# Kernel tuning notes

Hardware: AMD Instinct MI355X
Metric: run time of the kernel (lower is better)

## Reference

```python
import jax, jax.numpy as jnp
import numpy as np

B, N = 512, 128
NFEAT, NHID, NHEADS, HID = 133, 60, 8, 300
FP_DIM, FP2, TASK = 1489, 512, 1
ALPHA = 0.2
NEG = -9e15


def _lin(k, fi, fo):
    s = 1.0 / np.sqrt(fi)
    return jax.random.uniform(k, (fi, fo), minval=-s, maxval=s, dtype=jnp.float32)


def _vec(k, fi, n):
    s = 1.0 / np.sqrt(fi)
    return jax.random.uniform(k, (n,), minval=-s, maxval=s, dtype=jnp.float32)


def setup_inputs() -> dict:
    key = jax.random.key(0)
    ks = jax.random.split(key, 24)
    x = jax.random.normal(ks[0], (B, N, NFEAT), dtype=jnp.float32)
    adj = jax.random.randint(ks[1], (B, N, N), 0, 2, dtype=jnp.int32)
    adj = jnp.maximum(adj, jnp.eye(N, dtype=jnp.int32)[None])  # ensure valid softmax rows
    fp = jax.random.uniform(ks[2], (B, FP_DIM), dtype=jnp.float32)
    # multi-head GAT params (W has no bias; attention vector a split into src/dst halves)
    sW = 1.0 / np.sqrt(NFEAT)
    W_heads = jax.random.uniform(ks[3], (NHEADS, NFEAT, NHID), minval=-sW, maxval=sW, dtype=jnp.float32)
    sa = 1.0 / np.sqrt(2 * NHID)
    a_src = jax.random.uniform(ks[4], (NHEADS, NHID), minval=-sa, maxval=sa, dtype=jnp.float32)
    a_dst = jax.random.uniform(ks[5], (NHEADS, NHID), minval=-sa, maxval=sa, dtype=jnp.float32)
    W_out = _lin(ks[6], NHEADS * NHID, HID)
    ao_src = _vec(ks[7], 2 * HID, HID)
    ao_dst = _vec(ks[8], 2 * HID, HID)
    fc1_w = _lin(ks[9], FP_DIM, FP2); fc1_b = _vec(ks[10], FP_DIM, FP2)
    fc2_w = _lin(ks[11], FP2, HID); fc2_b = _vec(ks[12], FP2, HID)
    fcg_w = _lin(ks[13], HID, HID); fcg_b = _vec(ks[14], HID, HID)
    fcf_w = _lin(ks[15], HID, HID); fcf_b = _vec(ks[16], HID, HID)
    ffn1_w = _lin(ks[17], 2 * HID, HID); ffn1_b = _vec(ks[18], 2 * HID, HID)
    ffn2_w = _lin(ks[19], HID, TASK); ffn2_b = _vec(ks[20], HID, TASK)
    return {"x": x, "adj": adj, "fp": fp, "W_heads": W_heads, "a_src": a_src,
            "a_dst": a_dst, "W_out": W_out, "ao_src": ao_src, "ao_dst": ao_dst,
            "fc1_w": fc1_w, "fc1_b": fc1_b, "fc2_w": fc2_w, "fc2_b": fc2_b,
            "fcg_w": fcg_w, "fcg_b": fcg_b, "fcf_w": fcf_w, "fcf_b": fcf_b,
            "ffn1_w": ffn1_w, "ffn1_b": ffn1_b, "ffn2_w": ffn2_w, "ffn2_b": ffn2_b}


def reference(x, adj, fp, W_heads, a_src, a_dst, W_out, ao_src, ao_dst,
              fc1_w, fc1_b, fc2_w, fc2_b, fcg_w, fcg_b, fcf_w, fcf_b,
              ffn1_w, ffn1_b, ffn2_w, ffn2_b):
    adjm = adj > 0  # [B,N,N]
    # --- multi-head GAT layer (dropout = identity in eval) ---
    Wh = jnp.einsum('bnf,hfo->bhno', x, W_heads)              # [B,H,N,nhid]
    s = jnp.einsum('bhno,ho->bhn', Wh, a_src)
    d = jnp.einsum('bhno,ho->bhn', Wh, a_dst)
    # e_ij = leakyrelu(a . [Wh_i ; Wh_j]) without materializing [N,N,2F]
    e = jax.nn.leaky_relu(s[:, :, :, None] + d[:, :, None, :], ALPHA)
    e = jnp.where(adjm[:, None], e, NEG)
    att = jax.nn.softmax(e, axis=-1)                          # softmax over neighbors j
    hp = jax.nn.elu(jnp.einsum('bhnm,bhmo->bhno', att, Wh))   # concat=True head output
    h = hp.transpose(0, 2, 1, 3).reshape(B, N, NHEADS * NHID)
    # --- output GAT layer (concat=False) ---
    Wo = h @ W_out                                            # [B,N,HID]
    eo = jax.nn.leaky_relu((Wo @ ao_src)[:, :, None] + (Wo @ ao_dst)[:, None, :], ALPHA)
    eo = jnp.where(adjm, eo, NEG)
    ho = jax.nn.softmax(eo, axis=-1) @ Wo
    ho = jax.nn.log_softmax(jax.nn.elu(ho), axis=-1)          # log_softmax over features (dim=1 in torch)
    gat = ho.mean(axis=1)                                     # sum over atoms / atom_size
    # --- FPN branch ---
    f = jax.nn.relu(fp @ fc1_w + fc1_b)
    f = f @ fc2_w + fc2_b
    # --- fusion (gat_scale = 0.5) ---
    g = jax.nn.relu(gat @ fcg_w + fcg_b)
    f = jax.nn.relu(f @ fcf_w + fcf_b)
    z = jnp.concatenate([g, f], axis=1)                       # [B, 2*HID]
    z = jax.nn.relu(z @ ffn1_w + ffn1_b)
    z = z @ ffn2_w + ffn2_b
    return jax.nn.sigmoid(z)                                  # is_classif, eval mode
```

## Files before the change

### kernel.cpp

```cpp
#include <hip/hip_runtime.h>
#include <hip/hip_bf16.h>
#include <math.h>
#include <stdint.h>

#define LRA 0.2f

typedef __attribute__((ext_vector_type(8))) short bf16x8;
typedef __attribute__((ext_vector_type(8))) unsigned short u16x8;
typedef __attribute__((ext_vector_type(4))) float f32x4;
typedef unsigned long long u64;

__device__ __forceinline__ unsigned short f2bf(float v) {
  union { __hip_bfloat16 b; unsigned short u; } c;
  c.b = __float2bfloat16(v);
  return c.u;
}
__device__ __forceinline__ float bf2f(unsigned short h) {
  union { float f; unsigned int u; } a; a.u = ((unsigned int)h) << 16;
  return a.f;
}
__device__ __forceinline__ float warp_sum(float v){
  #pragma unroll
  for (int s = 32; s; s >>= 1) v += __shfl_xor(v, s);
  return v;
}

__global__ __launch_bounds__(256) void k_mask(const int* __restrict__ adj, u64* __restrict__ mg){
  const int t = threadIdx.x, lane = t & 63, w = t >> 6, b = blockIdx.x;
  const int* adjb = adj + (size_t)b * 128 * 128;
  for (int i = w * 32; i < w * 32 + 32; ++i) {
    u64 b0 = __ballot(adjb[i * 128 + lane] > 0);
    u64 b1 = __ballot(adjb[i * 128 + 64 + lane] > 0);
    if (lane == 0) { mg[((size_t)b * 128 + i) * 2] = b0; mg[((size_t)b * 128 + i) * 2 + 1] = b1; }
  }
}

__global__ __launch_bounds__(64) void k_prep1(
    const float* __restrict__ Whw, unsigned short* __restrict__ BH, unsigned short* __restrict__ BL)
{
  const int kt = blockIdx.x, nt = blockIdx.y, l = threadIdx.x;
  const int n = nt * 16 + (l & 15), k0 = kt * 32 + (l >> 4) * 8;
  const int hd = n >> 6, j = n & 63;
  uint4 hv, lv;
  unsigned int* hp = (unsigned int*)&hv;
  unsigned int* lp = (unsigned int*)&lv;
  #pragma unroll
  for (int p = 0; p < 4; ++p) {
    unsigned short hh[2], ll[2];
    #pragma unroll
    for (int e = 0; e < 2; ++e) {
      const int k = k0 + p * 2 + e;
      const float v = (j < 60 && k < 133) ? Whw[((size_t)hd * 133 + k) * 60 + j] : 0.f;
      const unsigned short h = f2bf(v);
      hh[e] = h; ll[e] = f2bf(v - bf2f(h));
    }
    hp[p] = hh[0] | ((unsigned int)hh[1] << 16);
    lp[p] = ll[0] | ((unsigned int)ll[1] << 16);
  }
  const size_t off = (((size_t)(kt * 32 + nt)) * 64 + l) * 8;
  *(uint4*)&BH[off] = hv;
  *(uint4*)&BL[off] = lv;
}

__global__ __launch_bounds__(64) void k_prep2(
    const float* __restrict__ W, unsigned short* __restrict__ BH, unsigned short* __restrict__ BL)
{
  const int kt = blockIdx.x, nt = blockIdx.y, l = threadIdx.x;
  const int n = nt * 16 + (l & 15), k0 = kt * 32 + (l >> 4) * 8;
  uint4 hv, lv;
  unsigned int* hp = (unsigned int*)&hv;
  unsigned int* lp = (unsigned int*)&lv;
  #pragma unroll
  for (int p = 0; p < 4; ++p) {
    unsigned short hh[2], ll[2];
    #pragma unroll
    for (int e = 0; e < 2; ++e) {
      const int k = k0 + p * 2 + e;
      const float v = (n < 300 && k < 480) ? W[(size_t)k * 300 + n] : 0.f;
      const unsigned short h = f2bf(v);
      hh[e] = h; ll[e] = f2bf(v - bf2f(h));
    }
    hp[p] = hh[0] | ((unsigned int)hh[1] << 16);
    lp[p] = ll[0] | ((unsigned int)ll[1] << 16);
  }
  const size_t off = (((size_t)(kt * 20 + nt)) * 64 + l) * 8;
  *(uint4*)&BH[off] = hv;
  *(uint4*)&BL[off] = lv;
}

__device__ __forceinline__ float make_att_frags(
    const float si, const u64 ma, const u64 mb2, const float* darr,
    const int g, bf16x8* pah, bf16x8* pal)
{
  const unsigned int mby[4] = {
    (unsigned int)(ma  >> (g * 8)) & 0xffu,
    (unsigned int)(ma  >> (32 + g * 8)) & 0xffu,
    (unsigned int)(mb2 >> (g * 8)) & 0xffu,
    (unsigned int)(mb2 >> (32 + g * 8)) & 0xffu };
  float ev[4][8];
  float mx = -3e38f;
  #pragma unroll
  for (int kt = 0; kt < 4; ++kt)
    #pragma unroll
    for (int e = 0; e < 8; ++e) {
      const int j = ((kt & 1) * 32) + ((kt >> 1) * 64) + g * 8 + e;
      float v = si + darr[j];
      v = fmaxf(v, LRA * v);
      const float vv = (mby[((kt & 1) << 1) | (kt >> 1)] & (1u << e)) ? v : -3e38f;
      ev[kt][e] = vv;
      mx = fmaxf(mx, vv);
    }
  mx = fmaxf(mx, __shfl_xor(mx, 16));
  mx = fmaxf(mx, __shfl_xor(mx, 32));
  float sum = 0.f;
  #pragma unroll
  for (int kt = 0; kt < 4; ++kt)
    #pragma unroll
    for (int e = 0; e < 8; ++e) {
      const float p = (ev[kt][e] > -1e37f) ? __expf(ev[kt][e] - mx) : 0.f;
      ev[kt][e] = p;
      sum += p;
    }
  sum += __shfl_xor(sum, 16);
  sum += __shfl_xor(sum, 32);
  #pragma unroll
  for (int kt = 0; kt < 4; ++kt) {
    const int ks = ((kt & 1) << 1) | (kt >> 1);
    union { unsigned int u[4]; bf16x8 v; } hw, lw;
    #pragma unroll
    for (int p2 = 0; p2 < 4; ++p2) {
      const float p0 = ev[ks][2 * p2], p1 = ev[ks][2 * p2 + 1];
      const unsigned short h0 = f2bf(p0), h1 = f2bf(p1);
      hw.u[p2] = h0 | ((unsigned int)h1 << 16);
      lw.u[p2] = f2bf(p0 - bf2f(h0)) | ((unsigned int)f2bf(p1 - bf2f(h1)) << 16);
    }
    pah[kt] = hw.v;
    pal[kt] = lw.v;
  }
  return 1.f / sum;
}

__global__ __launch_bounds__(512) void k_fga1(
    const float* __restrict__ x,
    const unsigned short* __restrict__ BH, const unsigned short* __restrict__ BL,
    const float* __restrict__ asrc, const float* __restrict__ adst,
    const u64* __restrict__ mg, unsigned int* __restrict__ buf1)
{
  __shared__ unsigned int Apk[128][32];
  __shared__ unsigned int Whp[64][132];
  __shared__ float asl[64], adl[64];
  __shared__ float sarr[128], darr[128];
  __shared__ u64 mAr[128], mBr[128];
  const int t = threadIdx.x, lane = t & 63, w = t >> 6, r = lane & 15, g = lane >> 4;
  const int hd = blockIdx.x >> 9, b = blockIdx.x & 511;
  const float* xb = x + (size_t)b * 128 * 133;
  unsigned int* slab = buf1 + (size_t)b * 61440;

  if (t < 64) {
    asl[t] = (t < 60) ? asrc[hd * 60 + t] : 0.f;
    adl[t] = (t < 60) ? adst[hd * 60 + t] : 0.f;
  }
  if (t < 128) {
    mAr[t] = mg[((size_t)b * 128 + t) * 2];
    mBr[t] = mg[((size_t)b * 128 + t) * 2 + 1];
  }

  f32x4 acc[4];
  #pragma unroll
  for (int ntl = 0; ntl < 4; ++ntl) acc[ntl] = (f32x4){0.f,0.f,0.f,0.f};

  for (int kt = 0; kt < 5; ++kt) {
    #pragma unroll
    for (int i = 0; i < 2; ++i) {
      const int idx = t + i * 512, row_l = idx >> 3, sl = idx & 7;
      const int k0 = kt * 32 + sl * 4;
      uint4 pk;
      unsigned int* pp = (unsigned int*)&pk;
      #pragma unroll
      for (int e = 0; e < 4; ++e) {
        const int k = k0 + e;
        const float v = (k < 133) ? xb[(size_t)row_l * 133 + k] : 0.f;
        const unsigned short h = f2bf(v);
        pp[e] = ((unsigned int)h << 16) | f2bf(v - bf2f(h));
      }
      *(uint4*)&Apk[row_l][((sl ^ (row_l & 7)) << 2)] = pk;
    }
    bf16x8 bh[4], bl[4];
    #pragma unroll
    for (int ntl = 0; ntl < 4; ++ntl) {
      const size_t off = (((size_t)(kt * 32 + hd * 4 + ntl)) * 64 + lane) * 8;
      bh[ntl] = *(const bf16x8*)&BH[off];
      bl[ntl] = *(const bf16x8*)&BL[off];
    }
    __syncthreads();
    {
      const int row_l = w * 16 + r, key = r & 7;
      const uint4 p0 = *(const uint4*)&Apk[row_l][(((2*g)   ^ key) << 2)];
      const uint4 p1 = *(const uint4*)&Apk[row_l][(((2*g+1) ^ key) << 2)];
      const unsigned int pw[8] = {p0.x,p0.y,p0.z,p0.w,p1.x,p1.y,p1.z,p1.w};
      bf16x8 ah, al;
      #pragma unroll
      for (int e = 0; e < 8; ++e) { ah[e] = (short)(pw[e] >> 16); al[e] = (short)(pw[e] & 0xffffu); }
      #pragma unroll
      for (int ntl = 0; ntl < 4; ++ntl) {
        acc[ntl] = __builtin_amdgcn_mfma_f32_16x16x32_bf16(ah, bh[ntl], acc[ntl], 0,0,0);
        acc[ntl] = __builtin_amdgcn_mfma_f32_16x16x32_bf16(al, bh[ntl], acc[ntl], 0,0,0);
        acc[ntl] = __builtin_amdgcn_mfma_f32_16x16x32_bf16(ah, bl[ntl], acc[ntl], 0,0,0);
      }
    }
    __syncthreads();
  }

  {
    float sv[4] = {0,0,0,0}, dv[4] = {0,0,0,0};
    #pragma unroll
    for (int ntl = 0; ntl < 4; ++ntl) {
      const int cl = ntl * 16 + r;
      const float as = asl[cl], ad = adl[cl];
      #pragma unroll
      for (int q = 0; q < 4; ++q) { sv[q] += acc[ntl][q] * as; dv[q] += acc[ntl][q] * ad; }
    }
    #pragma unroll
    for (int q = 0; q < 4; ++q) {
      #pragma unroll
      for (int s = 1; s <= 8; s <<= 1) { sv[q] += __shfl_xor(sv[q], s); dv[q] += __shfl_xor(dv[q], s); }
    }
    if (r == 0) {
      #pragma unroll
      for (int q = 0; q < 4; ++q) {
        sarr[w * 16 + g * 4 + q] = sv[q];
        darr[w * 16 + g * 4 + q] = dv[q];
      }
    }
  }
  #pragma unroll
  for (int ntl = 0; ntl < 4; ++ntl) {
    const int c = ntl * 16 + r;
    uint4 pv;
    unsigned int* pp = (unsigned int*)&pv;
    #pragma unroll
    for (int q = 0; q < 4; ++q) {
      const float v = acc[ntl][q];
      const unsigned short h = f2bf(v);
      pp[q] = ((unsigned int)h << 16) | f2bf(v - bf2f(h));
    }
    *(uint4*)&Whp[c][w * 16 + (g << 2)] = pv;
  }
  __syncthreads();

  bf16x8 pah[4], pal[4];
  const float inv = make_att_frags(sarr[w * 16 + r], mAr[w * 16 + r], mBr[w * 16 + r],
                                   darr, g, pah, pal);
  f32x4 pacc[4];
  #pragma unroll
  for (int ntl = 0; ntl < 4; ++ntl) pacc[ntl] = (f32x4){0.f,0.f,0.f,0.f};
  #pragma unroll
  for (int kt = 0; kt < 4; ++kt) {
    #pragma unroll
    for (int ntl = 0; ntl < 4; ++ntl) {
      const int c = ntl * 16 + r;
      const uint4 q0 = *(const uint4*)&Whp[c][kt * 32 + g * 8];
      const uint4 q1 = *(const uint4*)&Whp[c][kt * 32 + g * 8 + 4];
      const unsigned int pw[8] = {q0.x,q0.y,q0.z,q0.w,q1.x,q1.y,q1.z,q1.w};
      bf16x8 bh, bl;
      #pragma unroll
      for (int e = 0; e < 8; ++e) { bh[e] = (short)(pw[e] >> 16); bl[e] = (short)(pw[e] & 0xffffu); }
      pacc[ntl] = __builtin_amdgcn_mfma_f32_16x16x32_bf16(pah[kt], bh, pacc[ntl], 0,0,0);
      pacc[ntl] = __builtin_amdgcn_mfma_f32_16x16x32_bf16(pal[kt], bh, pacc[ntl], 0,0,0);
      pacc[ntl] = __builtin_amdgcn_mfma_f32_16x16x32_bf16(pah[kt], bl, pacc[ntl], 0,0,0);
    }
  }
  {
    float sc[4];
    #pragma unroll
    for (int q = 0; q < 4; ++q) sc[q] = __shfl(inv, g * 4 + q);
    #pragma unroll
    for (int ntl = 0; ntl < 4; ++ntl) {
      const int cc = ntl * 16 + r;
      if (cc < 60) {
        #pragma unroll
        for (int q = 0; q < 4; ++q) {
          const int row = w * 16 + g * 4 + q;
          float v = pacc[ntl][q] * sc[q];
          v = v > 0.f ? v : __expf(v) - 1.f;
          const unsigned short h = f2bf(v), l = f2bf(v - bf2f(h));
          slab[(size_t)hd * 7680 + (size_t)row * 60 + cc] = ((unsigned int)h << 16) | l;
        }
      }
    }
  }
}

__global__ __launch_bounds__(256, 3) void k_gemm2(
    unsigned int* __restrict__ buf1,
    const unsigned short* __restrict__ BH, const unsigned short* __restrict__ BL)
{
  __shared__ unsigned int Apk[64][32];
  const int t = threadIdx.x, lane = t & 63, w = t >> 6, r = lane & 15, g = lane >> 4;
  const int b = blockIdx.x >> 1, p = blockIdx.x & 1;
  const int row0 = p * 64;
  unsigned int* slab = buf1 + (size_t)b * 61440;

  f32x4 acc[4][5];
  #pragma unroll
  for (int mt = 0; mt < 4; ++mt)
    #pragma unroll
    for (int ntl = 0; ntl < 5; ++ntl) acc[mt][ntl] = (f32x4){0.f,0.f,0.f,0.f};

  for (int kt = 0; kt < 15; ++kt) {
    #pragma unroll
    for (int i = 0; i < 2; ++i) {
      const int idx = t + i * 256, row_l = idx >> 3, sl = idx & 7;
      const int k0 = kt * 32 + sl * 4;
      const int hd = k0 / 60, c = k0 - hd * 60;
      const uint4 v = *(const uint4*)&slab[(size_t)hd * 7680 + (size_t)(row0 + row_l) * 60 + c];
      *(uint4*)&Apk[row_l][((sl ^ (row_l & 7)) << 2)] = v;
    }
    bf16x8 bh[5], bl[5];
    #pragma unroll
    for (int ntl = 0; ntl < 5; ++ntl) {
      const int nt = w * 5 + ntl;
      const size_t off = (((size_t)(kt * 20 + nt)) * 64 + lane) * 8;
      bh[ntl] = *(const bf16x8*)&BH[off];
      bl[ntl] = *(const bf16x8*)&BL[off];
    }
    __syncthreads();
    #pragma unroll
    for (int mt = 0; mt < 4; ++mt) {
      const int row_l = mt * 16 + r, key = r & 7;
      const uint4 p0 = *(const uint4*)&Apk[row_l][(((2*g)   ^ key) << 2)];
      const uint4 p1 = *(const uint4*)&Apk[row_l][(((2*g+1) ^ key) << 2)];
      const unsigned int pw[8] = {p0.x,p0.y,p0.z,p0.w,p1.x,p1.y,p1.z,p1.w};
      bf16x8 ah, al;
      #pragma unroll
      for (int e = 0; e < 8; ++e) { ah[e] = (short)(pw[e] >> 16); al[e] = (short)(pw[e] & 0xffffu); }
      #pragma unroll
      for (int ntl = 0; ntl < 5; ++ntl) {
        acc[mt][ntl] = __builtin_amdgcn_mfma_f32_16x16x32_bf16(ah, bh[ntl], acc[mt][ntl], 0,0,0);
        acc[mt][ntl] = __builtin_amdgcn_mfma_f32_16x16x32_bf16(al, bh[ntl], acc[mt][ntl], 0,0,0);
        acc[mt][ntl] = __builtin_amdgcn_mfma_f32_16x16x32_bf16(ah, bl[ntl], acc[mt][ntl], 0,0,0);
      }
    }
    __syncthreads();
  }
  #pragma unroll
  for (int mt = 0; mt < 4; ++mt)
    #pragma unroll
    for (int ntl = 0; ntl < 5; ++ntl) {
      const int cc = w * 80 + ntl * 16 + r;
      if (cc < 300) {
        uint4 pv;
        unsigned int* pp = (unsigned int*)&pv;
        #pragma unroll
        for (int q = 0; q < 4; ++q) {
          const float v = acc[mt][ntl][q];
          const unsigned short h = f2bf(v);
          pp[q] = ((unsigned int)h << 16) | f2bf(v - bf2f(h));
        }
        *(uint4*)&slab[(size_t)cc * 128 + row0 + mt * 16 + (g << 2)] = pv;
      }
    }
}

__global__ __launch_bounds__(128) void k_sd2(
    const unsigned int* __restrict__ buf1, const float* __restrict__ aos,
    const float* __restrict__ aod, float* __restrict__ s2g, float* __restrict__ d2g)
{
  const int j = threadIdx.x, b = blockIdx.x;
  const unsigned int* slab = buf1 + (size_t)b * 61440;
  float s = 0.f, d = 0.f;
  #pragma unroll 4
  for (int c = 0; c < 300; ++c) {
    const float ac = aos[c], dc = aod[c];
    const unsigned int pk = slab[(size_t)c * 128 + j];
    const float v = bf2f((unsigned short)(pk >> 16)) + bf2f((unsigned short)(pk & 0xffffu));
    s += v * ac; d += v * dc;
  }
  s2g[(size_t)b * 128 + j] = s;
  d2g[(size_t)b * 128 + j] = d;
}

__global__ __launch_bounds__(256) void k_att2(
    const unsigned int* __restrict__ buf1, const u64* __restrict__ mg,
    const float* __restrict__ s2g, const float* __restrict__ d2g,
    float* __restrict__ gat)
{
  __shared__ unsigned short Th[16][64][8], Tl[16][64][8];
  __shared__ float sarr[128], darr[128];
  __shared__ u64 mAr[128], mBr[128];
  __shared__ float colsum[304];
  __shared__ float srow[16];
  const int t = threadIdx.x, lane = t & 63, w = t >> 6, r = lane & 15, g = lane >> 4;
  const int b = blockIdx.x;
  const unsigned int* slab = buf1 + (size_t)b * 61440;

  if (t < 128) {
    sarr[t] = s2g[(size_t)b * 128 + t];
    darr[t] = d2g[(size_t)b * 128 + t];
    mAr[t] = mg[((size_t)b * 128 + t) * 2];
    mBr[t] = mg[((size_t)b * 128 + t) * 2 + 1];
  }
  for (int c = t; c < 304; c += 256) colsum[c] = 0.f;
  __syncthreads();
  bf16x8 pah[2][4], pal[2][4];
  float inv2[2];
  #pragma unroll
  for (int mt = 0; mt < 2; ++mt) {
    const int i = w * 32 + mt * 16 + r;
    inv2[mt] = make_att_frags(sarr[i], mAr[i], mBr[i], darr, g, pah[mt], pal[mt]);
  }
  float scq[2][4];
  #pragma unroll
  for (int mt = 0; mt < 2; ++mt)
    #pragma unroll
    for (int q = 0; q < 4; ++q) scq[mt][q] = __shfl(inv2[mt], g * 4 + q);

  float m8[2][4], l8[2][4];
  #pragma unroll
  for (int mt = 0; mt < 2; ++mt)
    #pragma unroll
    for (int q = 0; q < 4; ++q) { m8[mt][q] = -3e38f; l8[mt][q] = 0.f; }

  for (int ch = 0; ch < 5; ++ch) {
    #pragma unroll
    for (int ii = 0; ii < 4; ++ii) {
      const int idx = t + ii * 256;
      const int c = idx & 63, jg = idx >> 6;
      const int gc = ch * 64 + c;
      uint4 p0 = {0,0,0,0}, p1 = {0,0,0,0};
      if (gc < 300) {
        const uint4* src = (const uint4*)&slab[(size_t)gc * 128 + jg * 8];
        p0 = src[0]; p1 = src[1];
      }
      const unsigned int pw[8] = {p0.x,p0.y,p0.z,p0.w,p1.x,p1.y,p1.z,p1.w};
      u16x8 hv, lv;
      #pragma unroll
      for (int e = 0; e < 8; ++e) { hv[e] = (unsigned short)(pw[e] >> 16); lv[e] = (unsigned short)(pw[e] & 0xffffu); }
      const int tile = ((c >> 4) << 2) | (jg >> 2);
      const int li = ((jg & 3) << 4) | (c & 15);
      *(u16x8*)&Th[tile][li][0] = hv;
      *(u16x8*)&Tl[tile][li][0] = lv;
    }
    __syncthreads();
    f32x4 pacc[2][4];
    #pragma unroll
    for (int mt = 0; mt < 2; ++mt)
      #pragma unroll
      for (int nt = 0; nt < 4; ++nt) pacc[mt][nt] = (f32x4){0.f,0.f,0.f,0.f};
    #pragma unroll
    for (int kt = 0; kt < 4; ++kt)
      #pragma unroll
      for (int nt = 0; nt < 4; ++nt) {
        const bf16x8 bh = *(const bf16x8*)&Th[(nt << 2) | kt][lane][0];
        const bf16x8 bl = *(const bf16x8*)&Tl[(nt << 2) | kt][lane][0];
        #pragma unroll
        for (int mt = 0; mt < 2; ++mt) {
          pacc[mt][nt] = __builtin_amdgcn_mfma_f32_16x16x32_bf16(pah[mt][kt], bh, pacc[mt][nt], 0,0,0);
          pacc[mt][nt] = __builtin_amdgcn_mfma_f32_16x16x32_bf16(pal[mt][kt], bh, pacc[mt][nt], 0,0,0);
          pacc[mt][nt] = __builtin_amdgcn_mfma_f32_16x16x32_bf16(pah[mt][kt], bl, pacc[mt][nt], 0,0,0);
        }
      }
    float csA[4] = {0,0,0,0};
    #pragma unroll
    for (int mt = 0; mt < 2; ++mt) {
      float vq[4][4];
      #pragma unroll
      for (int nt = 0; nt < 4; ++nt) {
        const int cc = ch * 64 + nt * 16 + r;
        const bool cv = cc < 300;
        #pragma unroll
        for (int q = 0; q < 4; ++q) {
          float v = pacc[mt][nt][q] * scq[mt][q];
          v = v > 0.f ? v : __expf(v) - 1.f;
          vq[nt][q] = cv ? v : -3e38f;
          csA[nt] += cv ? v : 0.f;
        }
      }
      #pragma unroll
      for (int q = 0; q < 4; ++q) {
        float mx = fmaxf(fmaxf(vq[0][q], vq[1][q]), fmaxf(vq[2][q], vq[3][q]));
        mx = fmaxf(mx, __shfl_xor(mx, 1));
        mx = fmaxf(mx, __shfl_xor(mx, 2));
        mx = fmaxf(mx, __shfl_xor(mx, 4));
        mx = fmaxf(mx, __shfl_xor(mx, 8));
        const float nm = fmaxf(m8[mt][q], mx);
        float ps = __expf(vq[0][q]-nm) + __expf(vq[1][q]-nm) + __expf(vq[2][q]-nm) + __expf(vq[3][q]-nm);
        ps += __shfl_xor(ps, 1); ps += __shfl_xor(ps, 2);
        ps += __shfl_xor(ps, 4); ps += __shfl_xor(ps, 8);
        l8[mt][q] = l8[mt][q] * __expf(m8[mt][q] - nm) + ps;
        m8[mt][q] = nm;
      }
    }
    #pragma unroll
    for (int nt = 0; nt < 4; ++nt) {
      float cs = csA[nt];
      cs += __shfl_xor(cs, 16); cs += __shfl_xor(cs, 32);
      const int cc = ch * 64 + nt * 16 + r;
      if (g == 0 && cc < 300) atomicAdd(&colsum[cc], cs);
    }
    __syncthreads();
  }
  if (r == 0) {
    float sp = 0.f;
    #pragma unroll
    for (int mt = 0; mt < 2; ++mt)
      #pragma unroll
      for (int q = 0; q < 4; ++q) sp += m8[mt][q] + __logf(l8[mt][q]);
    srow[w * 4 + g] = sp;
  }
  __syncthreads();
  float S = 0.f;
  #pragma unroll
  for (int k = 0; k < 16; ++k) S += srow[k];
  for (int c = t; c < 300; c += 256)
    gat[(size_t)b * 300 + c] = (colsum[c] - S) * (1.f / 128.f);
}

__global__ __launch_bounds__(256) void k_gemm_sk(
    const float* __restrict__ A, const float* __restrict__ B,
    float* __restrict__ P, int M, int K, int N, int kpt)
{
  __shared__ unsigned short Ah[64][40], Al[64][40], Bh[64][40], Bl[64][40];
  const int t = threadIdx.x, lane = t & 63, w = t >> 6, r = lane & 15, g = lane >> 4;
  const int row0 = blockIdx.x * 64, col0 = blockIdx.y * 64;
  const int sk = blockIdx.z;
  const int k0 = sk * kpt * 32;
  const int kend = min(K, k0 + kpt * 32);

  f32x4 acc[4];
  #pragma unroll
  for (int nt = 0; nt < 4; ++nt) acc[nt] = (f32x4){0.f,0.f,0.f,0.f};

  for (int kt = k0; kt < kend; kt += 32) {
    #pragma unroll
    for (int ii = 0; ii < 2; ++ii) {
      const int idx = t + ii * 256, ar = idx >> 3, aq = (idx & 7) * 4, gk = kt + aq;
      const float* ap = &A[(size_t)(row0 + ar) * K + gk];
      float v0 = gk     < kend ? ap[0] : 0.f;
      float v1 = gk + 1 < kend ? ap[1] : 0.f;
      float v2 = gk + 2 < kend ? ap[2] : 0.f;
      float v3 = gk + 3 < kend ? ap[3] : 0.f;
      unsigned short h0=f2bf(v0),h1=f2bf(v1),h2=f2bf(v2),h3=f2bf(v3);
      *(unsigned int*)&Ah[ar][aq]   = h0 | ((unsigned int)h1 << 16);
      *(unsigned int*)&Ah[ar][aq+2] = h2 | ((unsigned int)h3 << 16);
      unsigned short l0=f2bf(v0-bf2f(h0)),l1=f2bf(v1-bf2f(h1)),l2=f2bf(v2-bf2f(h2)),l3=f2bf(v3-bf2f(h3));
      *(unsigned int*)&Al[ar][aq]   = l0 | ((unsigned int)l1 << 16);
      *(unsigned int*)&Al[ar][aq+2] = l2 | ((unsigned int)l3 << 16);
    }
    #pragma unroll
    for (int ii = 0; ii < 4; ++ii) {
      const int idx = t + ii * 256, n = idx & 63, kk = (idx >> 6) * 2;
      const int gn = col0 + n;
      float v0 = (gn < N && kt + kk     < kend) ? B[(size_t)(kt + kk) * N + gn] : 0.f;
      float v1 = (gn < N && kt + kk + 1 < kend) ? B[(size_t)(kt + kk + 1) * N + gn] : 0.f;
      unsigned short h0 = f2bf(v0), h1 = f2bf(v1);
      *(unsigned int*)&Bh[n][kk] = h0 | ((unsigned int)h1 << 16);
      unsigned short l0 = f2bf(v0 - bf2f(h0)), l1 = f2bf(v1 - bf2f(h1));
      *(unsigned int*)&Bl[n][kk] = l0 | ((unsigned int)l1 << 16);
    }
    __syncthreads();
    const bf16x8 ah  = *(const bf16x8*)&Ah[w * 16 + r][g * 8];
    const bf16x8 al2 = *(const bf16x8*)&Al[w * 16 + r][g * 8];
    #pragma unroll
    for (int nt = 0; nt < 4; ++nt) {
      const bf16x8 bh = *(const bf16x8*)&Bh[nt * 16 + r][g * 8];
      const bf16x8 bl = *(const bf16x8*)&Bl[nt * 16 + r][g * 8];
      acc[nt] = __builtin_amdgcn_mfma_f32_16x16x32_bf16(ah,  bh, acc[nt], 0,0,0);
      acc[nt] = __builtin_amdgcn_mfma_f32_16x16x32_bf16(al2, bh, acc[nt], 0,0,0);
      acc[nt] = __builtin_amdgcn_mfma_f32_16x16x32_bf16(ah,  bl, acc[nt], 0,0,0);
    }
    __syncthreads();
  }
  float* Pout = P + (size_t)sk * M * N;
  #pragma unroll
  for (int nt = 0; nt < 4; ++nt) {
    const int cc = col0 + nt * 16 + r;
    if (cc < N) {
      #pragma unroll
      for (int q = 0; q < 4; ++q)
        Pout[(size_t)(row0 + w * 16 + g * 4 + q) * N + cc] = acc[nt][q];
    }
  }
}

__global__ __launch_bounds__(256) void k_reduce(
    const float* __restrict__ P, const float* __restrict__ bias,
    float* __restrict__ C, int M, int N, int ldc, int nsk, int act)
{
  const int idx = blockIdx.x * 256 + threadIdx.x;
  if (idx >= M * N) return;
  const int row = idx / N, col = idx - row * N;
  float s = bias[col];
  for (int k = 0; k < nsk; ++k) s += P[(size_t)k * M * N + idx];
  if (act) s = fmaxf(s, 0.f);
  C[(size_t)row * ldc + col] = s;
}

__global__ __launch_bounds__(512) void k_out(
    const float* __restrict__ z1, const float* __restrict__ w2,
    const float* __restrict__ b2, float* __restrict__ out)
{
  const int t = threadIdx.x, lane = t & 63, w = t >> 6;
  const int b = blockIdx.x * 8 + w;
  float p = 0.f;
  for (int k = lane; k < 300; k += 64) p += z1[(size_t)b * 300 + k] * w2[k];
  p = warp_sum(p);
  if (lane == 0) out[b] = 1.f / (1.f + __expf(-(p + b2[0])));
}

extern "C" void kernel_launch(void* const* d_in, const int* in_sizes, int n_in,
                              void* d_out, int out_size, void* d_ws, size_t ws_size,
                              hipStream_t stream)
{
  const float* x    = (const float*)d_in[0];
  const int*   adj  = (const int*)d_in[1];
  const float* fp   = (const float*)d_in[2];
  const float* Whw  = (const float*)d_in[3];
  const float* asrc = (const float*)d_in[4];
  const float* adst = (const float*)d_in[5];
  const float* Wout = (const float*)d_in[6];
  const float* aos  = (const float*)d_in[7];
  const float* aod  = (const float*)d_in[8];
  const float* fc1w = (const float*)d_in[9];
  const float* fc1b = (const float*)d_in[10];
  const float* fc2w = (const float*)d_in[11];
  const float* fc2b = (const float*)d_in[12];
  const float* fcgw = (const float*)d_in[13];
  const float* fcgb = (const float*)d_in[14];
  const float* fcfw = (const float*)d_in[15];
  const float* fcfb = (const float*)d_in[16];
  const float* f1w  = (const float*)d_in[17];
  const float* f1b  = (const float*)d_in[18];
  const float* f2w  = (const float*)d_in[19];
  const float* f2b  = (const float*)d_in[20];
  float* out = (float*)d_out;

  char* wsb = (char*)d_ws;
  unsigned int* buf1 = (unsigned int*)wsb;
  float* s2g = (float*)(wsb + 130023424);
  float* d2g = (float*)(wsb + 130285568);
  u64*   mgb = (u64*)  (wsb + 130547712);
  float* gatp = (float*)(wsb + 131596288);
  float* fpnp = (float*)(wsb + 132210688);
  float* f1buf = (float*)(wsb + 132825088);
  float* zb    = (float*)(wsb + 133873664);
  float* z1b   = (float*)(wsb + 135102464);
  float* P0 = (float*)(wsb + 135716864);
  float* P1 = (float*)(wsb + 142008320);
  float* P2 = (float*)(wsb + 144465920);
  float* P3 = (float*)(wsb + 145694720);
  float* P4 = (float*)(wsb + 146923520);
  unsigned short* Bf1H = (unsigned short*)(wsb + 149381120);
  unsigned short* Bf1L = (unsigned short*)(wsb + 149544960);
  unsigned short* Bf2H = (unsigned short*)(wsb + 149708800);
  unsigned short* Bf2L = (unsigned short*)(wsb + 150016000);

  k_prep1<<<dim3(5, 32), 64, 0, stream>>>(Whw, Bf1H, Bf1L);
  k_prep2<<<dim3(15, 20), 64, 0, stream>>>(Wout, Bf2H, Bf2L);
  k_mask <<<512, 256, 0, stream>>>(adj, mgb);
  k_fga1 <<<4096, 512, 0, stream>>>(x, Bf1H, Bf1L, asrc, adst, mgb, buf1);
  k_gemm2<<<1024, 256, 0, stream>>>(buf1, Bf2H, Bf2L);
  k_sd2  <<<512, 128, 0, stream>>>(buf1, aos, aod, s2g, d2g);
  k_att2 <<<512, 256, 0, stream>>>(buf1, mgb, s2g, d2g, gatp);
  k_gemm_sk<<<dim3(8,8,6), 256, 0, stream>>>(fp, fc1w, P0, 512, 1489, 512, 8);
  k_reduce<<<1024, 256, 0, stream>>>(P0, fc1b, f1buf, 512, 512, 512, 6, 1);
  k_gemm_sk<<<dim3(8,5,4), 256, 0, stream>>>(f1buf, fc2w, P1, 512, 512, 300, 4);
  k_reduce<<<600, 256, 0, stream>>>(P1, fc2b, fpnp, 512, 300, 300, 4, 0);
  k_gemm_sk<<<dim3(8,5,2), 256, 0, stream>>>(gatp, fcgw, P2, 512, 300, 300, 5);
  k_gemm_sk<<<dim3(8,5,2), 256, 0, stream>>>(fpnp, fcfw, P3, 512, 300, 300, 5);
  k_reduce<<<600, 256, 0, stream>>>(P2, fcgb, zb, 512, 300, 600, 2, 1);
  k_reduce<<<600, 256, 0, stream>>>(P3, fcfb, zb + 300, 512, 300, 600, 2, 1);
  k_gemm_sk<<<dim3(8,5,4), 256, 0, stream>>>(zb, f1w, P4, 512, 600, 300, 5);
  k_reduce<<<600, 256, 0, stream>>>(P4, f1b, z1b, 512, 300, 300, 4, 1);
  k_out<<<64, 512, 0, stream>>>(z1b, f2w, f2b, out);
}
```

Before: 385.9 us.

## Pre-split x into bf16 hi/lo arrays and store Wh in MFMA fragment layout

```diff
diff --git a/kernel.cpp b/kernel.cpp
--- a/kernel.cpp
+++ b/kernel.cpp
@@ -35,6 +35,27 @@
   }
 }
 
+__global__ __launch_bounds__(256) void k_prepx(
+    const float* __restrict__ x, unsigned short* __restrict__ xh, unsigned short* __restrict__ xl)
+{
+  const int b = blockIdx.x, t = threadIdx.x;
+  const float* xb = x + (size_t)b * 128 * 133;
+  for (int i = t; i < 4352; i += 256) {
+    const int row = i / 34, sl = i - (i / 34) * 34, k0 = sl * 4;
+    unsigned short hh[4], ll[4];
+    #pragma unroll
+    for (int e = 0; e < 4; ++e) {
+      const int k = k0 + e;
+      const float v = (k < 133) ? xb[(size_t)row * 133 + k] : 0.f;
+      const unsigned short h = f2bf(v);
+      hh[e] = h; ll[e] = f2bf(v - bf2f(h));
+    }
+    const size_t off = ((size_t)b * 128 + row) * 136 + k0;
+    *(uint2*)&xh[off] = *(const uint2*)hh;
+    *(uint2*)&xl[off] = *(const uint2*)ll;
+  }
+}
+
 __global__ __launch_bounds__(64) void k_prep1(
     const float* __restrict__ Whw, unsigned short* __restrict__ BH, unsigned short* __restrict__ BL)
 {
@@ -141,20 +162,22 @@
 }
 
 __global__ __launch_bounds__(512) void k_fga1(
-    const float* __restrict__ x,
+    const unsigned short* __restrict__ xh, const unsigned short* __restrict__ xl,
     const unsigned short* __restrict__ BH, const unsigned short* __restrict__ BL,
     const float* __restrict__ asrc, const float* __restrict__ adst,
     const u64* __restrict__ mg, unsigned int* __restrict__ buf1)
 {
-  __shared__ unsigned int Apk[128][32];
-  __shared__ unsigned int Whp[64][132];
+  __shared__ unsigned short SMEM[16384];
   __shared__ float asl[64], adl[64];
   __shared__ float sarr[128], darr[128];
   __shared__ u64 mAr[128], mBr[128];
   const int t = threadIdx.x, lane = t & 63, w = t >> 6, r = lane & 15, g = lane >> 4;
   const int hd = blockIdx.x >> 9, b = blockIdx.x & 511;
-  const float* xb = x + (size_t)b * 128 * 133;
   unsigned int* slab = buf1 + (size_t)b * 61440;
+  unsigned short* Ah = SMEM;
+  unsigned short* Al = SMEM + 5120;
+  unsigned short* Th = SMEM;
+  unsigned short* Tl = SMEM + 8192;
 
   if (t < 64) {
     asl[t] = (t < 60) ? asrc[hd * 60 + t] : 0.f;
@@ -170,20 +193,11 @@
   for (int ntl = 0; ntl < 4; ++ntl) acc[ntl] = (f32x4){0.f,0.f,0.f,0.f};
 
   for (int kt = 0; kt < 5; ++kt) {
-    #pragma unroll
-    for (int i = 0; i < 2; ++i) {
-      const int idx = t + i * 512, row_l = idx >> 3, sl = idx & 7;
-      const int k0 = kt * 32 + sl * 4;
-      uint4 pk;
-      unsigned int* pp = (unsigned int*)&pk;
-      #pragma unroll
-      for (int e = 0; e < 4; ++e) {
-        const int k = k0 + e;
-        const float v = (k < 133) ? xb[(size_t)row_l * 133 + k] : 0.f;
-        const unsigned short h = f2bf(v);
-        pp[e] = ((unsigned int)h << 16) | f2bf(v - bf2f(h));
-      }
-      *(uint4*)&Apk[row_l][((sl ^ (row_l & 7)) << 2)] = pk;
+    {
+      const int row = t >> 2, sl = t & 3;
+      const size_t src = ((size_t)b * 128 + row) * 136 + kt * 32 + sl * 8;
+      *(uint4*)&Ah[row * 40 + sl * 8] = *(const uint4*)&xh[src];
+      *(uint4*)&Al[row * 40 + sl * 8] = *(const uint4*)&xl[src];
     }
     bf16x8 bh[4], bl[4];
     #pragma unroll
@@ -194,13 +208,9 @@
     }
     __syncthreads();
     {
-      const int row_l = w * 16 + r, key = r & 7;
-      const uint4 p0 = *(const uint4*)&Apk[row_l][(((2*g)   ^ key) << 2)];
-      const uint4 p1 = *(const uint4*)&Apk[row_l][(((2*g+1) ^ key) << 2)];
-      const unsigned int pw[8] = {p0.x,p0.y,p0.z,p0.w,p1.x,p1.y,p1.z,p1.w};
-      bf16x8 ah, al;
-      #pragma unroll
-      for (int e = 0; e < 8; ++e) { ah[e] = (short)(pw[e] >> 16); al[e] = (short)(pw[e] & 0xffffu); }
+      const int row = w * 16 + r;
+      const bf16x8 ah = *(const bf16x8*)&Ah[row * 40 + g * 8];
+      const bf16x8 al = *(const bf16x8*)&Al[row * 40 + g * 8];
       #pragma unroll
       for (int ntl = 0; ntl < 4; ++ntl) {
         acc[ntl] = __builtin_amdgcn_mfma_f32_16x16x32_bf16(ah, bh[ntl], acc[ntl], 0,0,0);
@@ -235,16 +245,17 @@
   }
   #pragma unroll
   for (int ntl = 0; ntl < 4; ++ntl) {
-    const int c = ntl * 16 + r;
-    uint4 pv;
-    unsigned int* pp = (unsigned int*)&pv;
     #pragma unroll
     for (int q = 0; q < 4; ++q) {
+      const int gq = g * 4 + q;
+      const int tile = (ntl << 2) | (w >> 1);
+      const int li = (((w << 1) + (gq >> 3)) & 3) * 16 + r;
+      const int e = gq & 7;
       const float v = acc[ntl][q];
       const unsigned short h = f2bf(v);
-      pp[q] = ((unsigned int)h << 16) | f2bf(v - bf2f(h));
-    }
-    *(uint4*)&Whp[c][w * 16 + (g << 2)] = pv;
+      Th[((size_t)tile * 64 + li) * 8 + e] = h;
+      Tl[((size_t)tile * 64 + li) * 8 + e] = f2bf(v - bf2f(h));
+    }
   }
   __syncthreads();
 
@@ -258,13 +269,8 @@
   for (int kt = 0; kt < 4; ++kt) {
     #pragma unroll
     for (int ntl = 0; ntl < 4; ++ntl) {
-      const int c = ntl * 16 + r;
-      const uint4 q0 = *(const uint4*)&Whp[c][kt * 32 + g * 8];
-      const uint4 q1 = *(const uint4*)&Whp[c][kt * 32 + g * 8 + 4];
-      const unsigned int pw[8] = {q0.x,q0.y,q0.z,q0.w,q1.x,q1.y,q1.z,q1.w};
-      bf16x8 bh, bl;
-      #pragma unroll
-      for (int e = 0; e < 8; ++e) { bh[e] = (short)(pw[e] >> 16); bl[e] = (short)(pw[e] & 0xffffu); }
+      const bf16x8 bh = *(const bf16x8*)&Th[(((ntl << 2) | kt) * 64 + lane) * 8];
+      const bf16x8 bl = *(const bf16x8*)&Tl[(((ntl << 2) | kt) * 64 + lane) * 8];
       pacc[ntl] = __builtin_amdgcn_mfma_f32_16x16x32_bf16(pah[kt], bh, pacc[ntl], 0,0,0);
       pacc[ntl] = __builtin_amdgcn_mfma_f32_16x16x32_bf16(pal[kt], bh, pacc[ntl], 0,0,0);
       pacc[ntl] = __builtin_amdgcn_mfma_f32_16x16x32_bf16(pah[kt], bl, pacc[ntl], 0,0,0);
@@ -654,11 +660,14 @@
   unsigned short* Bf1L = (unsigned short*)(wsb + 149544960);
   unsigned short* Bf2H = (unsigned short*)(wsb + 149708800);
   unsigned short* Bf2L = (unsigned short*)(wsb + 150016000);
-
+  unsigned short* xh   = (unsigned short*)(wsb + 150323200);
+  unsigned short* xl   = (unsigned short*)(wsb + 168148992);
+
+  k_prepx<<<512, 256, 0, stream>>>(x, xh, xl);
   k_prep1<<<dim3(5, 32), 64, 0, stream>>>(Whw, Bf1H, Bf1L);
   k_prep2<<<dim3(15, 20), 64, 0, stream>>>(Wout, Bf2H, Bf2L);
   k_mask <<<512, 256, 0, stream>>>(adj, mgb);
-  k_fga1 <<<4096, 512, 0, stream>>>(x, Bf1H, Bf1L, asrc, adst, mgb, buf1);
+  k_fga1 <<<4096, 512, 0, stream>>>(xh, xl, Bf1H, Bf1L, asrc, adst, mgb, buf1);
   k_gemm2<<<1024, 256, 0, stream>>>(buf1, Bf2H, Bf2L);
   k_sd2  <<<512, 128, 0, stream>>>(buf1, aos, aod, s2g, d2g);
   k_att2 <<<512, 256, 0, stream>>>(buf1, mgb, s2g, d2g, gatp);
```

Measured after the change: 391.6 us. About the same (+1.5%).
